# Kernel tuning notes

Measured on AMD Instinct MI355X. Metric: run time of the kernel, lower is better.

The kernel has to match this reference:

```python
import jax, jax.numpy as jnp
import numpy as np

N_NODES = 50000
N_EDGES = 800000
D = 64
IN_DIM = 100
N_GRAPHS = 512
N_LAYERS = 3
OUT_DIM = 24  # n_lbs * n_tasks
BN_EPS = 1e-5


def setup_inputs() -> dict:
    key = jax.random.key(0)
    ks = iter(jax.random.split(key, 40))

    def w(shape):
        fan_in = shape[0]
        return jax.random.normal(next(ks), shape, jnp.float32) / np.float32(np.sqrt(fan_in))

    inp = {}
    inp["x"] = jax.random.normal(next(ks), (N_NODES, IN_DIM), jnp.float32)
    inp["edge_index"] = jax.random.randint(next(ks), (2, N_EDGES), 0, N_NODES, jnp.int32)
    inp["batch"] = jnp.sort(jax.random.randint(next(ks), (N_NODES,), 0, N_GRAPHS, jnp.int32))

    dims_in = [IN_DIM, D, D]
    for i in range(N_LAYERS):
        inp[f"w1_{i}"] = w((dims_in[i], D))
        inp[f"b1_{i}"] = jnp.zeros((D,), jnp.float32)
        inp[f"w2_{i}"] = w((D, D))
        inp[f"b2_{i}"] = jnp.zeros((D,), jnp.float32)

    inp["jk_w"] = w((N_LAYERS * D, D))
    inp["jk_b"] = jnp.zeros((D,), jnp.float32)
    inp["ffn_w1"] = w((D, D))
    inp["ffn_b1"] = jnp.zeros((D,), jnp.float32)
    inp["bn_g"] = jnp.ones((D,), jnp.float32)
    inp["bn_b"] = jnp.zeros((D,), jnp.float32)
    inp["bn_m"] = 0.1 * jax.random.normal(next(ks), (D,), jnp.float32)
    inp["bn_v"] = jax.random.uniform(next(ks), (D,), jnp.float32, 0.5, 1.5)
    inp["ffn_w2"] = w((D, D))
    inp["ffn_b2"] = jnp.zeros((D,), jnp.float32)
    inp["out_w"] = w((D, OUT_DIM))
    inp["out_b"] = jnp.zeros((OUT_DIM,), jnp.float32)
    return inp


def _gin_conv(h, src, dst, w1, b1, w2, b2):
    # sum-aggregate neighbor messages:  agg[dst] += h[src]
    agg = jax.ops.segment_sum(h[src], dst, num_segments=N_NODES)
    z = h + agg  # eps = 0 -> (1 + eps) * x + agg
    # GINConv internal MLP: lin -> relu -> lin (no norm, plain last)
    return jnp.maximum(z @ w1 + b1, 0.0) @ w2 + b2


def reference(x, edge_index, batch,
              w1_0, b1_0, w2_0, b2_0,
              w1_1, b1_1, w2_1, b2_1,
              w1_2, b1_2, w2_2, b2_2,
              jk_w, jk_b,
              ffn_w1, ffn_b1, bn_g, bn_b, bn_m, bn_v, ffn_w2, ffn_b2,
              out_w, out_b):
    src, dst = edge_index[0], edge_index[1]
    layer_params = [(w1_0, b1_0, w2_0, b2_0),
                    (w1_1, b1_1, w2_1, b2_1),
                    (w1_2, b1_2, w2_2, b2_2)]
    xs = []
    h = x
    for (w1, b1, w2, b2) in layer_params:
        h = _gin_conv(h, src, dst, w1, b1, w2, b2)
        h = jnp.maximum(h, 0.0)  # inter-layer ReLU (jk='cat' applies it on every layer)
        xs.append(h)  # dropout is identity in eval
    # JumpingKnowledge 'cat' + final linear -> [N, D]
    h = jnp.concatenate(xs, axis=-1) @ jk_w + jk_b
    # global_add_pool -> [N_GRAPHS, D]
    g = jax.ops.segment_sum(h, batch, num_segments=N_GRAPHS)
    # ffn MLP: lin -> batchnorm (eval, running stats) -> relu -> lin
    t = g @ ffn_w1 + ffn_b1
    t = (t - bn_m) * jax.lax.rsqrt(bn_v + BN_EPS) * bn_g + bn_b
    t = jnp.maximum(t, 0.0) @ ffn_w2 + ffn_b2
    # output layer ('none' uncertainty): plain linear
    logits = t @ out_w + out_b
    return logits
```

## Files before the change

### kernel.cpp

```cpp
#include <hip/hip_runtime.h>

#define NN 50000
#define NE 800000
#define NG 512
#define INDIM 100
#define OUTD 24
#define LROW 72
#define XROW 136
#define CSR_CAP 64
#define NB 196
#define BSH 8
#define BCAP 5120
#define CURS 16
#define EPB 4096
#define B_WPREP 80
#define B_WPREP0 112
#define B_CNT0 308
#define B_GP0 692

typedef __attribute__((ext_vector_type(8))) short short8;
typedef __attribute__((ext_vector_type(4))) float floatx4;

__device__ inline float bf2f(unsigned short u) {
    unsigned v = (unsigned)u << 16;
    float f;
    __builtin_memcpy(&f, &v, 4);
    return f;
}
__device__ inline unsigned short f2bf(float f) {
    unsigned u;
    __builtin_memcpy(&u, &f, 4);
    u += 0x7fffu + ((u >> 16) & 1u);
    return (unsigned short)(u >> 16);
}


__global__ __launch_bounds__(256) void k_prep(const float* __restrict__ s0, const float* __restrict__ s1,
                                              const float* __restrict__ s2, const float* __restrict__ s3,
                                              const float* __restrict__ s4,
                                              const float* __restrict__ w1_0,
                                              unsigned short* __restrict__ wT,
                                              unsigned short* __restrict__ w0T,
                                              int* __restrict__ count,
                                              float* __restrict__ gp,
                                              int* __restrict__ cursor) {
    int b = blockIdx.x, tid = threadIdx.x;
    if (b < B_WPREP) {
        const float* srcs[5] = {s0, s1, s2, s3, s4};
        int id = b >> 4;
        int off = ((b & 15) << 8) + tid;
        int k = off >> 6, n = off & 63;
        wT[id * 4096 + n * 64 + k] = f2bf(srcs[id][k * 64 + n]);
    } else if (b < B_WPREP0) {
        int i = (b - B_WPREP) * 256 + tid;
        int n = i >> 7, k = i & 127;
        w0T[n * 128 + k] = (k < INDIM) ? f2bf(w1_0[k * 64 + n]) : 0;
    } else if (b < B_CNT0) {
        int i = (b - B_WPREP0) * 256 + tid;
        if (i < NN) count[i] = 0;
        if (i < NB * CURS) cursor[i] = 0;
    } else {
        int i = (b - B_CNT0) * 256 + tid;
        if (i < 3 * NG * 64) gp[i] = 0.f;
    }
}


__global__ __launch_bounds__(256) void k_fill_a(const int* __restrict__ ei,
                                                int* __restrict__ cursor,
                                                unsigned* __restrict__ pairs) {
    __shared__ int lcnt[NB];
    __shared__ int lbase[NB];
    int t = threadIdx.x;
    for (int i = t; i < NB; i += 256) lcnt[i] = 0;
    __syncthreads();
    unsigned e0 = blockIdx.x * EPB;
    unsigned short dv[16], sv[16];
    short bkt[16];
#pragma unroll
    for (int j = 0; j < 16; ++j) {
        unsigned e = e0 + j * 256u + t;
        if (e < NE) {
            int d = ei[NE + e];
            int s = ei[e];
            dv[j] = (unsigned short)d;
            sv[j] = (unsigned short)s;
            bkt[j] = (short)(d >> BSH);
            atomicAdd(&lcnt[bkt[j]], 1);
        } else {
            bkt[j] = -1;
        }
    }
    __syncthreads();
    for (int i = t; i < NB; i += 256) {
        lbase[i] = atomicAdd(&cursor[i * CURS], lcnt[i]);
        lcnt[i] = 0;
    }
    __syncthreads();
#pragma unroll
    for (int j = 0; j < 16; ++j) {
        if (bkt[j] >= 0) {
            int b = bkt[j];
            int p = lbase[b] + atomicAdd(&lcnt[b], 1);
            if (p < BCAP)
                pairs[(size_t)b * BCAP + p] = ((unsigned)dv[j] << 16) | (unsigned)sv[j];
        }
    }
}


__global__ __launch_bounds__(256) void k_fill_b(const unsigned* __restrict__ pairs,
                                                const int* __restrict__ cursor,
                                                int* __restrict__ count,
                                                int* __restrict__ csr) {
    __shared__ int lcnt[256];
    int t = threadIdx.x, b = blockIdx.x;
    lcnt[t] = 0;
    __syncthreads();
    int tot = min(cursor[b * CURS], BCAP);
    const unsigned* pp = pairs + (size_t)b * BCAP;
    for (int i = t; i < tot; i += 256) {
        unsigned pr = pp[i];
        int d = (int)(pr >> 16);
        int s = (int)(pr & 0xFFFFu);
        int pos = atomicAdd(&lcnt[d & 255], 1);
        if (pos < CSR_CAP) csr[(size_t)d * CSR_CAP + pos] = s;
    }
    __syncthreads();
    int node = (b << BSH) + t;
    if (node < NN) count[node] = lcnt[t];
}


__global__ __launch_bounds__(256) void k_pre0(const float* __restrict__ x,
                                              const unsigned short* __restrict__ w1T,
                                              unsigned short* __restrict__ y) {
    __shared__ __align__(16) unsigned short xs[64 * XROW];
    int tid = threadIdx.x;
    int base = blockIdx.x * 64;
    for (int i = tid; i < 64 * 128; i += 256) {
        int r = i >> 7, c = i & 127;
        int node = base + r;
        float v = (c < INDIM && node < NN) ? x[(size_t)node * INDIM + c] : 0.f;
        xs[r * XROW + c] = f2bf(v);
    }
    __syncthreads();
    int wave = tid >> 6, lane = tid & 63;
    int quad = lane >> 4, l15 = lane & 15;
#pragma unroll
    for (int nt = 0; nt < 4; ++nt) {
        floatx4 c = {0.f, 0.f, 0.f, 0.f};
#pragma unroll
        for (int kk = 0; kk < 4; ++kk) {
            short8 a = *(const short8*)&xs[(wave * 16 + l15) * XROW + kk * 32 + quad * 8];
            short8 bb = *(const short8*)&w1T[(nt * 16 + l15) * 128 + kk * 32 + quad * 8];
            c = __builtin_amdgcn_mfma_f32_16x16x32_bf16(a, bb, c, 0, 0, 0);
        }
        int col = nt * 16 + l15;
#pragma unroll
        for (int r = 0; r < 4; ++r) {
            int row = base + wave * 16 + quad * 4 + r;
            if (row < NN) y[(size_t)row * 64 + col] = f2bf(c[r]);
        }
    }
}


template <bool HAS_NEXT>
__global__ __launch_bounds__(256) void k_layer(const unsigned short* __restrict__ y,
                                               const int* __restrict__ count,
                                               const int* __restrict__ csr,
                                               const float* __restrict__ b1,
                                               const unsigned short* __restrict__ w2T,
                                               const float* __restrict__ b2,
                                               const unsigned short* __restrict__ wnT,
                                               unsigned short* __restrict__ ynext,
                                               const int* __restrict__ batch,
                                               float* __restrict__ gp) {
    __shared__ __align__(16) unsigned short tA[16 * LROW];
    __shared__ __align__(16) unsigned short tB[16 * LROW];
    int wave = threadIdx.x >> 6, lane = threadIdx.x & 63;
    int base = blockIdx.x * 16;
    float bias1 = b1[lane];

    for (int i = 0; i < 4; i += 2) {
        int nA = __builtin_amdgcn_readfirstlane(base + wave * 4 + i);
        int nB = __builtin_amdgcn_readfirstlane(base + wave * 4 + i + 1);
        int cA = min(count[nA], CSR_CAP);
        int cB = min(count[nB], CSR_CAP);
        const int* pA = csr + (size_t)nA * CSR_CAP;
        const int* pB = csr + (size_t)nB * CSR_CAP;
        float aA[4], aB[4];
        aA[0] = bf2f(y[(size_t)nA * 64 + lane]);
        aB[0] = bf2f(y[(size_t)nB * 64 + lane]);
        aA[1] = aA[2] = aA[3] = 0.f;
        aB[1] = aB[2] = aB[3] = 0.f;
        int eA = 0, eB = 0;
        while (eA + 8 <= cA && eB + 8 <= cB) {
            int iA[8], iB[8];
#pragma unroll
            for (int j = 0; j < 8; ++j) { iA[j] = pA[eA + j]; iB[j] = pB[eB + j]; }
            float vA[8], vB[8];
#pragma unroll
            for (int j = 0; j < 8; ++j) vA[j] = bf2f(y[(size_t)iA[j] * 64 + lane]);
#pragma unroll
            for (int j = 0; j < 8; ++j) vB[j] = bf2f(y[(size_t)iB[j] * 64 + lane]);
#pragma unroll
            for (int j = 0; j < 8; ++j) { aA[j & 3] += vA[j]; aB[j & 3] += vB[j]; }
            eA += 8; eB += 8;
        }
        for (; eA + 8 <= cA; eA += 8) {
            int idx[8];
#pragma unroll
            for (int j = 0; j < 8; ++j) idx[j] = pA[eA + j];
#pragma unroll
            for (int j = 0; j < 8; ++j) aA[j & 3] += bf2f(y[(size_t)idx[j] * 64 + lane]);
        }
        if (eA + 4 <= cA) {
            int i0 = pA[eA], i1 = pA[eA + 1], i2 = pA[eA + 2], i3 = pA[eA + 3];
            aA[0] += bf2f(y[(size_t)i0 * 64 + lane]);
            aA[1] += bf2f(y[(size_t)i1 * 64 + lane]);
            aA[2] += bf2f(y[(size_t)i2 * 64 + lane]);
            aA[3] += bf2f(y[(size_t)i3 * 64 + lane]);
            eA += 4;
        }
        if (eA + 2 <= cA) {
            int i0 = pA[eA], i1 = pA[eA + 1];
            aA[0] += bf2f(y[(size_t)i0 * 64 + lane]);
            aA[1] += bf2f(y[(size_t)i1 * 64 + lane]);
            eA += 2;
        }
        if (eA < cA) aA[0] += bf2f(y[(size_t)pA[eA] * 64 + lane]);
        for (; eB + 8 <= cB; eB += 8) {
            int idx[8];
#pragma unroll
            for (int j = 0; j < 8; ++j) idx[j] = pB[eB + j];
#pragma unroll
            for (int j = 0; j < 8; ++j) aB[j & 3] += bf2f(y[(size_t)idx[j] * 64 + lane]);
        }
        if (eB + 4 <= cB) {
            int i0 = pB[eB], i1 = pB[eB + 1], i2 = pB[eB + 2], i3 = pB[eB + 3];
            aB[0] += bf2f(y[(size_t)i0 * 64 + lane]);
            aB[1] += bf2f(y[(size_t)i1 * 64 + lane]);
            aB[2] += bf2f(y[(size_t)i2 * 64 + lane]);
            aB[3] += bf2f(y[(size_t)i3 * 64 + lane]);
            eB += 4;
        }
        if (eB + 2 <= cB) {
            int i0 = pB[eB], i1 = pB[eB + 1];
            aB[0] += bf2f(y[(size_t)i0 * 64 + lane]);
            aB[1] += bf2f(y[(size_t)i1 * 64 + lane]);
            eB += 2;
        }
        if (eB < cB) aB[0] += bf2f(y[(size_t)pB[eB] * 64 + lane]);

        float sA = (aA[0] + aA[1]) + (aA[2] + aA[3]);
        float sB = (aB[0] + aB[1]) + (aB[2] + aB[3]);
        tA[(wave * 4 + i) * LROW + lane]     = f2bf(fmaxf(sA + bias1, 0.f));
        tA[(wave * 4 + i + 1) * LROW + lane] = f2bf(fmaxf(sB + bias1, 0.f));
    }
    __syncthreads();

    int quad = lane >> 4, l15 = lane & 15;

    short8 a_k0 = *(const short8*)&tA[l15 * LROW + quad * 8];
    short8 a_k1 = *(const short8*)&tA[l15 * LROW + 32 + quad * 8];
    {
        int col = wave * 16 + l15;
        short8 b_k0 = *(const short8*)&w2T[col * 64 + quad * 8];
        short8 b_k1 = *(const short8*)&w2T[col * 64 + 32 + quad * 8];
        floatx4 c = {0.f, 0.f, 0.f, 0.f};
        c = __builtin_amdgcn_mfma_f32_16x16x32_bf16(a_k0, b_k0, c, 0, 0, 0);
        c = __builtin_amdgcn_mfma_f32_16x16x32_bf16(a_k1, b_k1, c, 0, 0, 0);
        float bb = b2[col];
#pragma unroll
        for (int r = 0; r < 4; ++r) {
            float h = fmaxf(c[r] + bb, 0.f);
            tB[(quad * 4 + r) * LROW + col] = f2bf(h);
        }
    }
    __syncthreads();

    if (wave == 0) {
        float run = 0.f;
        int curg = batch[base];
        for (int r = 0; r < 16; ++r) {
            int g2 = batch[base + r];
            if (g2 != curg) {
                atomicAdd(&gp[curg * 64 + lane], run);
                run = 0.f;
                curg = g2;
            }
            run += bf2f(tB[r * LROW + lane]);
        }
        atomicAdd(&gp[curg * 64 + lane], run);
    }

    if (HAS_NEXT) {
        short8 h_k0 = *(const short8*)&tB[l15 * LROW + quad * 8];
        short8 h_k1 = *(const short8*)&tB[l15 * LROW + 32 + quad * 8];
        int col = wave * 16 + l15;
        short8 w_k0 = *(const short8*)&wnT[col * 64 + quad * 8];
        short8 w_k1 = *(const short8*)&wnT[col * 64 + 32 + quad * 8];
        floatx4 cy = {0.f, 0.f, 0.f, 0.f};
        cy = __builtin_amdgcn_mfma_f32_16x16x32_bf16(h_k0, w_k0, cy, 0, 0, 0);
        cy = __builtin_amdgcn_mfma_f32_16x16x32_bf16(h_k1, w_k1, cy, 0, 0, 0);
#pragma unroll
        for (int r = 0; r < 4; ++r) {
            int row = base + quad * 4 + r;
            ynext[(size_t)row * 64 + col] = f2bf(cy[r]);
        }
    }
}


__device__ inline int lbound(const int* __restrict__ b, int v) {
    int lo = 0, hi = NN;
    while (lo < hi) {
        int m = (lo + hi) >> 1;
        if (b[m] < v) lo = m + 1; else hi = m;
    }
    return lo;
}

__global__ __launch_bounds__(64) void k_final(const float* __restrict__ gp,
                                              const int* __restrict__ batch,
                                              const float* __restrict__ jkw,
                                              const float* __restrict__ jkb,
                                              const float* __restrict__ w1,
                                              const float* __restrict__ b1,
                                              const float* __restrict__ bng,
                                              const float* __restrict__ bnb,
                                              const float* __restrict__ bnm,
                                              const float* __restrict__ bnv,
                                              const float* __restrict__ w2,
                                              const float* __restrict__ b2,
                                              const float* __restrict__ ow,
                                              const float* __restrict__ ob,
                                              float* __restrict__ out) {
    __shared__ float gs[192];
    __shared__ float gv[64];
    __shared__ float t2[64];
    __shared__ float t3[64];
    int gr = blockIdx.x, lane = threadIdx.x;
    gs[lane]       = gp[0 * NG * 64 + gr * 64 + lane];
    gs[64 + lane]  = gp[1 * NG * 64 + gr * 64 + lane];
    gs[128 + lane] = gp[2 * NG * 64 + gr * 64 + lane];
    float cntf = (float)(lbound(batch, gr + 1) - lbound(batch, gr));
    __syncthreads();
    float acc = cntf * jkb[lane];
#pragma unroll 8
    for (int k = 0; k < 192; ++k) acc = fmaf(gs[k], jkw[k * 64 + lane], acc);
    gv[lane] = acc;
    __syncthreads();
    acc = b1[lane];
#pragma unroll 8
    for (int k = 0; k < 64; ++k) acc = fmaf(gv[k], w1[k * 64 + lane], acc);
    acc = (acc - bnm[lane]) * rsqrtf(bnv[lane] + 1e-5f) * bng[lane] + bnb[lane];
    t2[lane] = fmaxf(acc, 0.f);
    __syncthreads();
    float acc2 = b2[lane];
#pragma unroll 8
    for (int k = 0; k < 64; ++k) acc2 = fmaf(t2[k], w2[k * 64 + lane], acc2);
    t3[lane] = acc2;
    __syncthreads();
    if (lane < OUTD) {
        float acc3 = ob[lane];
#pragma unroll 8
        for (int k = 0; k < 64; ++k) acc3 = fmaf(t3[k], ow[k * OUTD + lane], acc3);
        out[gr * OUTD + lane] = acc3;
    }
}

extern "C" void kernel_launch(void* const* d_in, const int* in_sizes, int n_in,
                              void* d_out, int out_size, void* d_ws, size_t ws_size,
                              hipStream_t stream) {
    const float* x     = (const float*)d_in[0];
    const int*   ei    = (const int*)d_in[1];
    const int*   batch = (const int*)d_in[2];
    const float* w1_0 = (const float*)d_in[3];
    const float* b1_0 = (const float*)d_in[4];
    const float* w2_0 = (const float*)d_in[5];
    const float* b2_0 = (const float*)d_in[6];
    const float* w1_1 = (const float*)d_in[7];
    const float* b1_1 = (const float*)d_in[8];
    const float* w2_1 = (const float*)d_in[9];
    const float* b2_1 = (const float*)d_in[10];
    const float* w1_2 = (const float*)d_in[11];
    const float* b1_2 = (const float*)d_in[12];
    const float* w2_2 = (const float*)d_in[13];
    const float* b2_2 = (const float*)d_in[14];
    const float* jk_w = (const float*)d_in[15];
    const float* jk_b = (const float*)d_in[16];
    const float* ffn_w1 = (const float*)d_in[17];
    const float* ffn_b1 = (const float*)d_in[18];
    const float* bn_g = (const float*)d_in[19];
    const float* bn_b = (const float*)d_in[20];
    const float* bn_m = (const float*)d_in[21];
    const float* bn_v = (const float*)d_in[22];
    const float* ffn_w2 = (const float*)d_in[23];
    const float* ffn_b2 = (const float*)d_in[24];
    const float* out_w  = (const float*)d_in[25];
    const float* out_b  = (const float*)d_in[26];

    float* ws = (float*)d_ws;
    unsigned short* ya = (unsigned short*)ws;
    unsigned short* yb = ya + 3200000;
    float* gp  = (float*)(yb + 3200000);
    int*   count = (int*)(gp + 3 * NG * 64);
    int*   csr   = count + NN;
    unsigned short* wT  = (unsigned short*)(csr + (size_t)NN * CSR_CAP);
    unsigned short* w0T = wT + 5 * 4096;
    int* cursor = (int*)(w0T + 64 * 128);
    unsigned* pairs = (unsigned*)(cursor + NB * CURS);

    k_prep<<<B_GP0, 256, 0, stream>>>(w2_0, w2_1, w2_2, w1_1, w1_2, w1_0,
                                      wT, w0T, count, gp, cursor);

    k_fill_a<<<(NE + EPB - 1) / EPB, 256, 0, stream>>>(ei, cursor, pairs);
    k_fill_b<<<NB, 256, 0, stream>>>(pairs, cursor, count, csr);

    k_pre0<<<(NN + 63) / 64, 256, 0, stream>>>(x, w0T, ya);

    int nblk = NN / 16;
    k_layer<true><<<nblk, 256, 0, stream>>>(ya, count, csr, b1_0,
                                            wT + 0 * 4096, b2_0, wT + 3 * 4096,
                                            yb, batch, gp + 0 * NG * 64);
    k_layer<true><<<nblk, 256, 0, stream>>>(yb, count, csr, b1_1,
                                            wT + 1 * 4096, b2_1, wT + 4 * 4096,
                                            ya, batch, gp + 1 * NG * 64);
    k_layer<false><<<nblk, 256, 0, stream>>>(ya, count, csr, b1_2,
                                             wT + 2 * 4096, b2_2, nullptr,
                                             nullptr, batch, gp + 2 * NG * 64);

    k_final<<<NG, 64, 0, stream>>>(gp, batch, jk_w, jk_b,
                                   ffn_w1, ffn_b1, bn_g, bn_b, bn_m, bn_v,
                                   ffn_w2, ffn_b2, out_w, out_b, (float*)d_out);
}
```

Measured before the change: 248.0 us.

## Fuse all stages into one persistent cooperative kernel with grid syncs

Replaces the seven separate kernel launches with a single cooperative persistent kernel that uses grid.sync between stages and atomic tile tickets for dynamic work distribution. Edge bucketing (fill_a) and the first-layer projection (pre0) now run in the same phase. The count-array zeroing is dropped because fill_b writes every count. This removes launch overhead and inter-kernel gaps. In exchange it pays for grid barriers, limits occupancy to co-resident blocks sharing one shared-memory footprint, and adds ticket atomics per tile.

```diff
diff --git a/kernel.cpp b/kernel.cpp
--- a/kernel.cpp
+++ b/kernel.cpp
@@ -1,4 +1,5 @@
 #include <hip/hip_runtime.h>
+#include <hip/hip_cooperative_groups.h>
 
 #define NN 50000
 #define NE 800000
@@ -13,13 +14,15 @@
 #define BCAP 5120
 #define CURS 16
 #define EPB 4096
-#define B_WPREP 80
-#define B_WPREP0 112
-#define B_CNT0 308
-#define B_GP0 692
+#define NT_PREP 497
+#define NT_P1 978
+#define NT_LAYER 3125
+#define NT_FINAL 128
 
 typedef __attribute__((ext_vector_type(8))) short short8;
 typedef __attribute__((ext_vector_type(4))) float floatx4;
+
+namespace cg = cooperative_groups;
 
 __device__ inline float bf2f(unsigned short u) {
     unsigned v = (unsigned)u << 16;
@@ -34,55 +37,59 @@
     return (unsigned short)(u >> 16);
 }
 
-
-__global__ __launch_bounds__(256) void k_prep(const float* __restrict__ s0, const float* __restrict__ s1,
-                                              const float* __restrict__ s2, const float* __restrict__ s3,
-                                              const float* __restrict__ s4,
-                                              const float* __restrict__ w1_0,
-                                              unsigned short* __restrict__ wT,
-                                              unsigned short* __restrict__ w0T,
-                                              int* __restrict__ count,
-                                              float* __restrict__ gp,
-                                              int* __restrict__ cursor) {
-    int b = blockIdx.x, tid = threadIdx.x;
-    if (b < B_WPREP) {
-        const float* srcs[5] = {s0, s1, s2, s3, s4};
-        int id = b >> 4;
-        int off = ((b & 15) << 8) + tid;
+struct Params {
+    const float* x;
+    const int* ei;
+    const int* batch;
+    const float *w2_0, *w2_1, *w2_2, *w1_1, *w1_2, *w1_0;
+    const float *b1_0, *b2_0, *b1_1, *b2_1, *b1_2, *b2_2;
+    const float *jkw, *jkb, *fw1, *fb1, *bng, *bnb, *bnm, *bnv, *fw2, *fb2, *ow, *ob;
+    float* out;
+    unsigned short *ya, *yb;
+    float* gp;
+    int* count;
+    int* csr;
+    unsigned short *wT, *w0T;
+    int* cursor;
+    unsigned* pairs;
+    int* tick;
+};
+
+
+__device__ __forceinline__ void prep_body(const Params& p, int u, int tid) {
+    if (u < 80) {
+        const float* srcs[5] = {p.w2_0, p.w2_1, p.w2_2, p.w1_1, p.w1_2};
+        int id = u >> 4;
+        int off = ((u & 15) << 8) + tid;
         int k = off >> 6, n = off & 63;
-        wT[id * 4096 + n * 64 + k] = f2bf(srcs[id][k * 64 + n]);
-    } else if (b < B_WPREP0) {
-        int i = (b - B_WPREP) * 256 + tid;
+        p.wT[id * 4096 + n * 64 + k] = f2bf(srcs[id][k * 64 + n]);
+    } else if (u < 112) {
+        int i = (u - 80) * 256 + tid;
         int n = i >> 7, k = i & 127;
-        w0T[n * 128 + k] = (k < INDIM) ? f2bf(w1_0[k * 64 + n]) : 0;
-    } else if (b < B_CNT0) {
-        int i = (b - B_WPREP0) * 256 + tid;
-        if (i < NN) count[i] = 0;
-        if (i < NB * CURS) cursor[i] = 0;
+        p.w0T[n * 128 + k] = (k < INDIM) ? f2bf(p.w1_0[k * 64 + n]) : 0;
+    } else if (u == 112) {
+        for (int i = tid; i < NB * CURS; i += 256) p.cursor[i] = 0;
+        if (tid < 4) p.tick[tid] = 0;
     } else {
-        int i = (b - B_CNT0) * 256 + tid;
-        if (i < 3 * NG * 64) gp[i] = 0.f;
-    }
-}
-
-
-__global__ __launch_bounds__(256) void k_fill_a(const int* __restrict__ ei,
-                                                int* __restrict__ cursor,
-                                                unsigned* __restrict__ pairs) {
-    __shared__ int lcnt[NB];
-    __shared__ int lbase[NB];
-    int t = threadIdx.x;
-    for (int i = t; i < NB; i += 256) lcnt[i] = 0;
-    __syncthreads();
-    unsigned e0 = blockIdx.x * EPB;
+        int i = (u - 113) * 256 + tid;
+        if (i < 3 * NG * 64) p.gp[i] = 0.f;
+    }
+}
+
+__device__ __forceinline__ void filla_body(const Params& p, int u, int tid, unsigned char* sm) {
+    int* lcnt = (int*)sm;
+    int* lbase = lcnt + NB;
+    for (int i = tid; i < NB; i += 256) lcnt[i] = 0;
+    __syncthreads();
+    unsigned e0 = (unsigned)u * EPB;
     unsigned short dv[16], sv[16];
     short bkt[16];
 #pragma unroll
     for (int j = 0; j < 16; ++j) {
-        unsigned e = e0 + j * 256u + t;
+        unsigned e = e0 + j * 256u + tid;
         if (e < NE) {
-            int d = ei[NE + e];
-            int s = ei[e];
+            int d = p.ei[NE + e];
+            int s = p.ei[e];
             dv[j] = (unsigned short)d;
             sv[j] = (unsigned short)s;
             bkt[j] = (short)(d >> BSH);
@@ -92,8 +99,8 @@
         }
     }
     __syncthreads();
-    for (int i = t; i < NB; i += 256) {
-        lbase[i] = atomicAdd(&cursor[i * CURS], lcnt[i]);
+    for (int i = tid; i < NB; i += 256) {
+        lbase[i] = atomicAdd(&p.cursor[i * CURS], lcnt[i]);
         lcnt[i] = 0;
     }
     __syncthreads();
@@ -101,98 +108,91 @@
     for (int j = 0; j < 16; ++j) {
         if (bkt[j] >= 0) {
             int b = bkt[j];
-            int p = lbase[b] + atomicAdd(&lcnt[b], 1);
-            if (p < BCAP)
-                pairs[(size_t)b * BCAP + p] = ((unsigned)dv[j] << 16) | (unsigned)sv[j];
-        }
-    }
-}
-
-
-__global__ __launch_bounds__(256) void k_fill_b(const unsigned* __restrict__ pairs,
-                                                const int* __restrict__ cursor,
-                                                int* __restrict__ count,
-                                                int* __restrict__ csr) {
-    __shared__ int lcnt[256];
-    int t = threadIdx.x, b = blockIdx.x;
-    lcnt[t] = 0;
-    __syncthreads();
-    int tot = min(cursor[b * CURS], BCAP);
-    const unsigned* pp = pairs + (size_t)b * BCAP;
-    for (int i = t; i < tot; i += 256) {
+            int pos = lbase[b] + atomicAdd(&lcnt[b], 1);
+            if (pos < BCAP)
+                p.pairs[(size_t)b * BCAP + pos] = ((unsigned)dv[j] << 16) | (unsigned)sv[j];
+        }
+    }
+    __syncthreads();
+}
+
+__device__ __forceinline__ void pre0_body(const Params& p, int v, int tid, unsigned char* sm) {
+    unsigned short* xs = (unsigned short*)sm;
+    int base = v * 64;
+    for (int i = tid; i < 64 * 128; i += 256) {
+        int r = i >> 7, c = i & 127;
+        int node = base + r;
+        float val = (c < INDIM && node < NN) ? p.x[(size_t)node * INDIM + c] : 0.f;
+        xs[r * XROW + c] = f2bf(val);
+    }
+    __syncthreads();
+    int wave = tid >> 6, lane = tid & 63;
+    int quad = lane >> 4, l15 = lane & 15;
+#pragma unroll
+    for (int nt = 0; nt < 4; ++nt) {
+        floatx4 c = {0.f, 0.f, 0.f, 0.f};
+#pragma unroll
+        for (int kk = 0; kk < 4; ++kk) {
+            short8 a = *(const short8*)&xs[(wave * 16 + l15) * XROW + kk * 32 + quad * 8];
+            short8 bb = *(const short8*)&p.w0T[(nt * 16 + l15) * 128 + kk * 32 + quad * 8];
+            c = __builtin_amdgcn_mfma_f32_16x16x32_bf16(a, bb, c, 0, 0, 0);
+        }
+        int col = nt * 16 + l15;
+#pragma unroll
+        for (int r = 0; r < 4; ++r) {
+            int row = base + wave * 16 + quad * 4 + r;
+            if (row < NN) p.ya[(size_t)row * 64 + col] = f2bf(c[r]);
+        }
+    }
+    __syncthreads();
+}
+
+__device__ __forceinline__ void fillb_body(const Params& p, int b, int tid, unsigned char* sm) {
+    int* lcnt = (int*)sm;
+    lcnt[tid] = 0;
+    __syncthreads();
+    int tot = min(p.cursor[b * CURS], BCAP);
+    const unsigned* pp = p.pairs + (size_t)b * BCAP;
+    for (int i = tid; i < tot; i += 256) {
         unsigned pr = pp[i];
         int d = (int)(pr >> 16);
         int s = (int)(pr & 0xFFFFu);
         int pos = atomicAdd(&lcnt[d & 255], 1);
-        if (pos < CSR_CAP) csr[(size_t)d * CSR_CAP + pos] = s;
-    }
-    __syncthreads();
-    int node = (b << BSH) + t;
-    if (node < NN) count[node] = lcnt[t];
-}
-
-
-__global__ __launch_bounds__(256) void k_pre0(const float* __restrict__ x,
-                                              const unsigned short* __restrict__ w1T,
-                                              unsigned short* __restrict__ y) {
-    __shared__ __align__(16) unsigned short xs[64 * XROW];
-    int tid = threadIdx.x;
-    int base = blockIdx.x * 64;
-    for (int i = tid; i < 64 * 128; i += 256) {
-        int r = i >> 7, c = i & 127;
-        int node = base + r;
-        float v = (c < INDIM && node < NN) ? x[(size_t)node * INDIM + c] : 0.f;
-        xs[r * XROW + c] = f2bf(v);
-    }
-    __syncthreads();
+        if (pos < CSR_CAP) p.csr[(size_t)d * CSR_CAP + pos] = s;
+    }
+    __syncthreads();
+    int node = (b << BSH) + tid;
+    if (node < NN) p.count[node] = lcnt[tid];
+    __syncthreads();
+}
+
+__device__ __forceinline__ void layer_body(const Params& p, int t, int tid,
+                                           const unsigned short* __restrict__ y,
+                                           const float* __restrict__ b1,
+                                           const unsigned short* __restrict__ w2T,
+                                           const float* __restrict__ b2,
+                                           const unsigned short* __restrict__ wnT,
+                                           unsigned short* __restrict__ ynext,
+                                           float* __restrict__ gp,
+                                           unsigned char* sm) {
+    unsigned short* tA = (unsigned short*)sm;
+    unsigned short* tB = tA + 16 * LROW;
     int wave = tid >> 6, lane = tid & 63;
-    int quad = lane >> 4, l15 = lane & 15;
-#pragma unroll
-    for (int nt = 0; nt < 4; ++nt) {
-        floatx4 c = {0.f, 0.f, 0.f, 0.f};
-#pragma unroll
-        for (int kk = 0; kk < 4; ++kk) {
-            short8 a = *(const short8*)&xs[(wave * 16 + l15) * XROW + kk * 32 + quad * 8];
-            short8 bb = *(const short8*)&w1T[(nt * 16 + l15) * 128 + kk * 32 + quad * 8];
-            c = __builtin_amdgcn_mfma_f32_16x16x32_bf16(a, bb, c, 0, 0, 0);
-        }
-        int col = nt * 16 + l15;
-#pragma unroll
-        for (int r = 0; r < 4; ++r) {
-            int row = base + wave * 16 + quad * 4 + r;
-            if (row < NN) y[(size_t)row * 64 + col] = f2bf(c[r]);
-        }
-    }
-}
-
-
-template <bool HAS_NEXT>
-__global__ __launch_bounds__(256) void k_layer(const unsigned short* __restrict__ y,
-                                               const int* __restrict__ count,
-                                               const int* __restrict__ csr,
-                                               const float* __restrict__ b1,
-                                               const unsigned short* __restrict__ w2T,
-                                               const float* __restrict__ b2,
-                                               const unsigned short* __restrict__ wnT,
-                                               unsigned short* __restrict__ ynext,
-                                               const int* __restrict__ batch,
-                                               float* __restrict__ gp) {
-    __shared__ __align__(16) unsigned short tA[16 * LROW];
-    __shared__ __align__(16) unsigned short tB[16 * LROW];
-    int wave = threadIdx.x >> 6, lane = threadIdx.x & 63;
-    int base = blockIdx.x * 16;
+    int base = t * 16;
     float bias1 = b1[lane];
+    const int* __restrict__ count = p.count;
+    const int* __restrict__ csr = p.csr;
 
     for (int i = 0; i < 4; i += 2) {
         int nA = __builtin_amdgcn_readfirstlane(base + wave * 4 + i);
-        int nB = __builtin_amdgcn_readfirstlane(base + wave * 4 + i + 1);
+        int nBn = __builtin_amdgcn_readfirstlane(base + wave * 4 + i + 1);
         int cA = min(count[nA], CSR_CAP);
-        int cB = min(count[nB], CSR_CAP);
+        int cB = min(count[nBn], CSR_CAP);
         const int* pA = csr + (size_t)nA * CSR_CAP;
-        const int* pB = csr + (size_t)nB * CSR_CAP;
+        const int* pB = csr + (size_t)nBn * CSR_CAP;
         float aA[4], aB[4];
         aA[0] = bf2f(y[(size_t)nA * 64 + lane]);
-        aB[0] = bf2f(y[(size_t)nB * 64 + lane]);
+        aB[0] = bf2f(y[(size_t)nBn * 64 + lane]);
         aA[1] = aA[2] = aA[3] = 0.f;
         aB[1] = aB[2] = aB[3] = 0.f;
         int eA = 0, eB = 0;
@@ -283,9 +283,9 @@
 
     if (wave == 0) {
         float run = 0.f;
-        int curg = batch[base];
+        int curg = p.batch[base];
         for (int r = 0; r < 16; ++r) {
-            int g2 = batch[base + r];
+            int g2 = p.batch[base + r];
             if (g2 != curg) {
                 atomicAdd(&gp[curg * 64 + lane], run);
                 run = 0.f;
@@ -296,7 +296,7 @@
         atomicAdd(&gp[curg * 64 + lane], run);
     }
 
-    if (HAS_NEXT) {
+    if (ynext) {
         short8 h_k0 = *(const short8*)&tB[l15 * LROW + quad * 8];
         short8 h_k1 = *(const short8*)&tB[l15 * LROW + 32 + quad * 8];
         int col = wave * 16 + l15;
@@ -311,8 +311,8 @@
             ynext[(size_t)row * 64 + col] = f2bf(cy[r]);
         }
     }
-}
-
+    __syncthreads();
+}
 
 __device__ inline int lbound(const int* __restrict__ b, int v) {
     int lo = 0, hi = NN;
@@ -323,117 +323,162 @@
     return lo;
 }
 
-__global__ __launch_bounds__(64) void k_final(const float* __restrict__ gp,
-                                              const int* __restrict__ batch,
-                                              const float* __restrict__ jkw,
-                                              const float* __restrict__ jkb,
-                                              const float* __restrict__ w1,
-                                              const float* __restrict__ b1,
-                                              const float* __restrict__ bng,
-                                              const float* __restrict__ bnb,
-                                              const float* __restrict__ bnm,
-                                              const float* __restrict__ bnv,
-                                              const float* __restrict__ w2,
-                                              const float* __restrict__ b2,
-                                              const float* __restrict__ ow,
-                                              const float* __restrict__ ob,
-                                              float* __restrict__ out) {
-    __shared__ float gs[192];
-    __shared__ float gv[64];
-    __shared__ float t2[64];
-    __shared__ float t3[64];
-    int gr = blockIdx.x, lane = threadIdx.x;
-    gs[lane]       = gp[0 * NG * 64 + gr * 64 + lane];
-    gs[64 + lane]  = gp[1 * NG * 64 + gr * 64 + lane];
-    gs[128 + lane] = gp[2 * NG * 64 + gr * 64 + lane];
-    float cntf = (float)(lbound(batch, gr + 1) - lbound(batch, gr));
-    __syncthreads();
-    float acc = cntf * jkb[lane];
+__device__ __forceinline__ void final_body(const Params& p, int u, int tid, unsigned char* sm) {
+    int wave = tid >> 6, lane = tid & 63;
+    int gr = u * 4 + wave;
+    float* gs = (float*)sm + wave * 384;
+    float* gv = gs + 192;
+    float* t2 = gv + 64;
+    float* t3 = t2 + 64;
+    gs[lane]       = p.gp[0 * NG * 64 + gr * 64 + lane];
+    gs[64 + lane]  = p.gp[1 * NG * 64 + gr * 64 + lane];
+    gs[128 + lane] = p.gp[2 * NG * 64 + gr * 64 + lane];
+    float cntf = (float)(lbound(p.batch, gr + 1) - lbound(p.batch, gr));
+    __syncthreads();
+    float acc = cntf * p.jkb[lane];
 #pragma unroll 8
-    for (int k = 0; k < 192; ++k) acc = fmaf(gs[k], jkw[k * 64 + lane], acc);
+    for (int k = 0; k < 192; ++k) acc = fmaf(gs[k], p.jkw[k * 64 + lane], acc);
     gv[lane] = acc;
     __syncthreads();
-    acc = b1[lane];
+    acc = p.fb1[lane];
 #pragma unroll 8
-    for (int k = 0; k < 64; ++k) acc = fmaf(gv[k], w1[k * 64 + lane], acc);
-    acc = (acc - bnm[lane]) * rsqrtf(bnv[lane] + 1e-5f) * bng[lane] + bnb[lane];
+    for (int k = 0; k < 64; ++k) acc = fmaf(gv[k], p.fw1[k * 64 + lane], acc);
+    acc = (acc - p.bnm[lane]) * rsqrtf(p.bnv[lane] + 1e-5f) * p.bng[lane] + p.bnb[lane];
     t2[lane] = fmaxf(acc, 0.f);
     __syncthreads();
-    float acc2 = b2[lane];
+    float acc2 = p.fb2[lane];
 #pragma unroll 8
-    for (int k = 0; k < 64; ++k) acc2 = fmaf(t2[k], w2[k * 64 + lane], acc2);
+    for (int k = 0; k < 64; ++k) acc2 = fmaf(t2[k], p.fw2[k * 64 + lane], acc2);
     t3[lane] = acc2;
     __syncthreads();
     if (lane < OUTD) {
-        float acc3 = ob[lane];
+        float acc3 = p.ob[lane];
 #pragma unroll 8
-        for (int k = 0; k < 64; ++k) acc3 = fmaf(t3[k], ow[k * OUTD + lane], acc3);
-        out[gr * OUTD + lane] = acc3;
-    }
+        for (int k = 0; k < 64; ++k) acc3 = fmaf(t3[k], p.ow[k * OUTD + lane], acc3);
+        p.out[gr * OUTD + lane] = acc3;
+    }
+}
+
+
+__global__ __launch_bounds__(256) void k_all(Params p) {
+    cg::grid_group grid = cg::this_grid();
+    __shared__ __align__(16) unsigned char sm[64 * XROW * 2];
+    __shared__ int sT;
+    int tid = threadIdx.x;
+    int nb = gridDim.x;
+    int bid = blockIdx.x;
+
+    for (int u = bid; u < NT_PREP; u += nb) prep_body(p, u, tid);
+    grid.sync();
+
+    {
+        if (bid < NT_P1) {
+            if (bid < NB) filla_body(p, bid, tid, sm);
+            else pre0_body(p, bid - NB, tid, sm);
+        }
+        if (nb < NT_P1) {
+            for (;;) {
+                __syncthreads();
+                if (tid == 0) sT = nb + atomicAdd(&p.tick[0], 1);
+                __syncthreads();
+                int t2 = sT;
+                if (t2 >= NT_P1) break;
+                if (t2 < NB) filla_body(p, t2, tid, sm);
+                else pre0_body(p, t2 - NB, tid, sm);
+            }
+        }
+    }
+    grid.sync();
+
+    for (int u = bid; u < NB; u += nb) fillb_body(p, u, tid, sm);
+    grid.sync();
+
+#pragma unroll 1
+    for (int l = 0; l < 3; ++l) {
+        const unsigned short* yin = (l == 1) ? p.yb : p.ya;
+        unsigned short* yout = (l == 0) ? p.yb : ((l == 1) ? p.ya : nullptr);
+        const unsigned short* w2T = p.wT + l * 4096;
+        const unsigned short* wnT = p.wT + (3 + l) * 4096;
+        const float* b1 = (l == 0) ? p.b1_0 : (l == 1) ? p.b1_1 : p.b1_2;
+        const float* b2 = (l == 0) ? p.b2_0 : (l == 1) ? p.b2_1 : p.b2_2;
+        float* gp = p.gp + l * NG * 64;
+        if (bid < NT_LAYER)
+            layer_body(p, bid, tid, yin, b1, w2T, b2, wnT, yout, gp, sm);
+        for (;;) {
+            __syncthreads();
+            if (tid == 0) sT = nb + atomicAdd(&p.tick[1 + l], 1);
+            __syncthreads();
+            int t2 = sT;
+            if (t2 >= NT_LAYER) break;
+            layer_body(p, t2, tid, yin, b1, w2T, b2, wnT, yout, gp, sm);
+        }
+        grid.sync();
+    }
+
+    if (bid < NT_FINAL) final_body(p, bid, tid, sm);
 }
 
 extern "C" void kernel_launch(void* const* d_in, const int* in_sizes, int n_in,
                               void* d_out, int out_size, void* d_ws, size_t ws_size,
                               hipStream_t stream) {
-    const float* x     = (const float*)d_in[0];
-    const int*   ei    = (const int*)d_in[1];
-    const int*   batch = (const int*)d_in[2];
-    const float* w1_0 = (const float*)d_in[3];
-    const float* b1_0 = (const float*)d_in[4];
-    const float* w2_0 = (const float*)d_in[5];
-    const float* b2_0 = (const float*)d_in[6];
-    const float* w1_1 = (const float*)d_in[7];
-    const float* b1_1 = (const float*)d_in[8];
-    const float* w2_1 = (const float*)d_in[9];
-    const float* b2_1 = (const float*)d_in[10];
-    const float* w1_2 = (const float*)d_in[11];
-    const float* b1_2 = (const float*)d_in[12];
-    const float* w2_2 = (const float*)d_in[13];
-    const float* b2_2 = (const float*)d_in[14];
-    const float* jk_w = (const float*)d_in[15];
-    const float* jk_b = (const float*)d_in[16];
-    const float* ffn_w1 = (const float*)d_in[17];
-    const float* ffn_b1 = (const float*)d_in[18];
-    const float* bn_g = (const float*)d_in[19];
-    const float* bn_b = (const float*)d_in[20];
-    const float* bn_m = (const float*)d_in[21];
-    const float* bn_v = (const float*)d_in[22];
-    const float* ffn_w2 = (const float*)d_in[23];
-    const float* ffn_b2 = (const float*)d_in[24];
-    const float* out_w  = (const float*)d_in[25];
-    const float* out_b  = (const float*)d_in[26];
+    Params p;
+    p.x     = (const float*)d_in[0];
+    p.ei    = (const int*)d_in[1];
+    p.batch = (const int*)d_in[2];
+    p.w1_0 = (const float*)d_in[3];
+    p.b1_0 = (const float*)d_in[4];
+    p.w2_0 = (const float*)d_in[5];
+    p.b2_0 = (const float*)d_in[6];
+    p.w1_1 = (const float*)d_in[7];
+    p.b1_1 = (const float*)d_in[8];
+    p.w2_1 = (const float*)d_in[9];
+    p.b2_1 = (const float*)d_in[10];
+    p.w1_2 = (const float*)d_in[11];
+    p.b1_2 = (const float*)d_in[12];
+    p.w2_2 = (const float*)d_in[13];
+    p.b2_2 = (const float*)d_in[14];
+    p.jkw  = (const float*)d_in[15];
+    p.jkb  = (const float*)d_in[16];
+    p.fw1  = (const float*)d_in[17];
+    p.fb1  = (const float*)d_in[18];
+    p.bng  = (const float*)d_in[19];
+    p.bnb  = (const float*)d_in[20];
+    p.bnm  = (const float*)d_in[21];
+    p.bnv  = (const float*)d_in[22];
+    p.fw2  = (const float*)d_in[23];
+    p.fb2  = (const float*)d_in[24];
+    p.ow   = (const float*)d_in[25];
+    p.ob   = (const float*)d_in[26];
+    p.out  = (float*)d_out;
 
     float* ws = (float*)d_ws;
-    unsigned short* ya = (unsigned short*)ws;
-    unsigned short* yb = ya + 3200000;
-    float* gp  = (float*)(yb + 3200000);
-    int*   count = (int*)(gp + 3 * NG * 64);
-    int*   csr   = count + NN;
-    unsigned short* wT  = (unsigned short*)(csr + (size_t)NN * CSR_CAP);
-    unsigned short* w0T = wT + 5 * 4096;
-    int* cursor = (int*)(w0T + 64 * 128);
-    unsigned* pairs = (unsigned*)(cursor + NB * CURS);
-
-    k_prep<<<B_GP0, 256, 0, stream>>>(w2_0, w2_1, w2_2, w1_1, w1_2, w1_0,
-                                      wT, w0T, count, gp, cursor);
-
-    k_fill_a<<<(NE + EPB - 1) / EPB, 256, 0, stream>>>(ei, cursor, pairs);
-    k_fill_b<<<NB, 256, 0, stream>>>(pairs, cursor, count, csr);
-
-    k_pre0<<<(NN + 63) / 64, 256, 0, stream>>>(x, w0T, ya);
-
-    int nblk = NN / 16;
-    k_layer<true><<<nblk, 256, 0, stream>>>(ya, count, csr, b1_0,
-                                            wT + 0 * 4096, b2_0, wT + 3 * 4096,
-                                            yb, batch, gp + 0 * NG * 64);
-    k_layer<true><<<nblk, 256, 0, stream>>>(yb, count, csr, b1_1,
-                                            wT + 1 * 4096, b2_1, wT + 4 * 4096,
-                                            ya, batch, gp + 1 * NG * 64);
-    k_layer<false><<<nblk, 256, 0, stream>>>(ya, count, csr, b1_2,
-                                             wT + 2 * 4096, b2_2, nullptr,
-                                             nullptr, batch, gp + 2 * NG * 64);
-
-    k_final<<<NG, 64, 0, stream>>>(gp, batch, jk_w, jk_b,
-                                   ffn_w1, ffn_b1, bn_g, bn_b, bn_m, bn_v,
-                                   ffn_w2, ffn_b2, out_w, out_b, (float*)d_out);
-}
+    p.ya = (unsigned short*)ws;
+    p.yb = p.ya + 3200000;
+    p.gp = (float*)(p.yb + 3200000);
+    p.count = (int*)(p.gp + 3 * NG * 64);
+    p.csr = p.count + NN;
+    p.wT = (unsigned short*)(p.csr + (size_t)NN * CSR_CAP);
+    p.w0T = p.wT + 5 * 4096;
+    p.cursor = (int*)(p.w0T + 64 * 128);
+    p.pairs = (unsigned*)(p.cursor + NB * CURS);
+    p.tick = (int*)(p.pairs + (size_t)NB * BCAP);
+
+    static int nblk_s = 0;
+    if (nblk_s == 0) {
+        int dev = 0;
+        hipGetDevice(&dev);
+        hipDeviceProp_t prop;
+        hipGetDeviceProperties(&prop, dev);
+        int mb = 0;
+        hipOccupancyMaxActiveBlocksPerMultiprocessor(&mb, reinterpret_cast<const void*>(k_all), 256, 0);
+        if (mb < 1) mb = 1;
+        long nb = (long)mb * prop.multiProcessorCount;
+        if (nb > 2048) nb = 2048;
+        if (nb < 256) nb = 256;
+        nblk_s = (int)nb;
+    }
+
+    void* args[] = { (void*)&p };
+    hipLaunchCooperativeKernel(reinterpret_cast<void*>(k_all),
+                               dim3(nblk_s), dim3(256), args, 0, stream);
+}
```

Result: slower. 768.8 us (+210.0%).

## Merge CSR fill with input projection; gather four nodes per wave with zero-row padding

Applied to the files above, without the earlier changes.

Merges the CSR-fill kernel and the first-layer input projection into one launch by giving them disjoint block ranges, which removes a launch and lets the two independent jobs overlap. The per-wave neighbour gather now handles four nodes at once in a single padded loop. Out-of-range slots read a zero row appended at index NN of each feature buffer, replacing the branchy tail code and raising loads in flight. This costs extra wasted loads when degrees within a wave differ, plus more register pressure.

```diff
diff --git a/kernel.cpp b/kernel.cpp
--- a/kernel.cpp
+++ b/kernel.cpp
@@ -8,6 +8,7 @@
 #define LROW 72
 #define XROW 136
 #define CSR_CAP 64
+#define YSZ 3200064
 #define NB 196
 #define BSH 8
 #define BCAP 5120
@@ -43,7 +44,9 @@
                                               unsigned short* __restrict__ w0T,
                                               int* __restrict__ count,
                                               float* __restrict__ gp,
-                                              int* __restrict__ cursor) {
+                                              int* __restrict__ cursor,
+                                              unsigned short* __restrict__ ya,
+                                              unsigned short* __restrict__ yb) {
     int b = blockIdx.x, tid = threadIdx.x;
     if (b < B_WPREP) {
         const float* srcs[5] = {s0, s1, s2, s3, s4};
@@ -59,6 +62,10 @@
         int i = (b - B_WPREP0) * 256 + tid;
         if (i < NN) count[i] = 0;
         if (i < NB * CURS) cursor[i] = 0;
+        if (i < 64) {
+            ya[(size_t)NN * 64 + i] = 0;
+            yb[(size_t)NN * 64 + i] = 0;
+        }
     } else {
         int i = (b - B_CNT0) * 256 + tid;
         if (i < 3 * NG * 64) gp[i] = 0.f;
@@ -109,35 +116,35 @@
 }
 
 
-__global__ __launch_bounds__(256) void k_fill_b(const unsigned* __restrict__ pairs,
-                                                const int* __restrict__ cursor,
-                                                int* __restrict__ count,
-                                                int* __restrict__ csr) {
-    __shared__ int lcnt[256];
-    int t = threadIdx.x, b = blockIdx.x;
-    lcnt[t] = 0;
-    __syncthreads();
-    int tot = min(cursor[b * CURS], BCAP);
-    const unsigned* pp = pairs + (size_t)b * BCAP;
-    for (int i = t; i < tot; i += 256) {
-        unsigned pr = pp[i];
-        int d = (int)(pr >> 16);
-        int s = (int)(pr & 0xFFFFu);
-        int pos = atomicAdd(&lcnt[d & 255], 1);
-        if (pos < CSR_CAP) csr[(size_t)d * CSR_CAP + pos] = s;
-    }
-    __syncthreads();
-    int node = (b << BSH) + t;
-    if (node < NN) count[node] = lcnt[t];
-}
-
-
-__global__ __launch_bounds__(256) void k_pre0(const float* __restrict__ x,
+__global__ __launch_bounds__(256) void k_mid2(const unsigned* __restrict__ pairs,
+                                              const int* __restrict__ cursor,
+                                              int* __restrict__ count,
+                                              int* __restrict__ csr,
+                                              const float* __restrict__ x,
                                               const unsigned short* __restrict__ w1T,
                                               unsigned short* __restrict__ y) {
     __shared__ __align__(16) unsigned short xs[64 * XROW];
     int tid = threadIdx.x;
-    int base = blockIdx.x * 64;
+    if (blockIdx.x < NB) {
+        int* lcnt = (int*)xs;
+        int b = blockIdx.x;
+        lcnt[tid] = 0;
+        __syncthreads();
+        int tot = min(cursor[b * CURS], BCAP);
+        const unsigned* pp = pairs + (size_t)b * BCAP;
+        for (int i = tid; i < tot; i += 256) {
+            unsigned pr = pp[i];
+            int d = (int)(pr >> 16);
+            int s = (int)(pr & 0xFFFFu);
+            int pos = atomicAdd(&lcnt[d & 255], 1);
+            if (pos < CSR_CAP) csr[(size_t)d * CSR_CAP + pos] = s;
+        }
+        __syncthreads();
+        int node = (b << BSH) + tid;
+        if (node < NN) count[node] = lcnt[tid];
+        return;
+    }
+    int base = (blockIdx.x - NB) * 64;
     for (int i = tid; i < 64 * 128; i += 256) {
         int r = i >> 7, c = i & 127;
         int node = base + r;
@@ -183,81 +190,73 @@
     int base = blockIdx.x * 16;
     float bias1 = b1[lane];
 
-    for (int i = 0; i < 4; i += 2) {
-        int nA = __builtin_amdgcn_readfirstlane(base + wave * 4 + i);
-        int nB = __builtin_amdgcn_readfirstlane(base + wave * 4 + i + 1);
-        int cA = min(count[nA], CSR_CAP);
-        int cB = min(count[nB], CSR_CAP);
-        const int* pA = csr + (size_t)nA * CSR_CAP;
-        const int* pB = csr + (size_t)nB * CSR_CAP;
-        float aA[4], aB[4];
-        aA[0] = bf2f(y[(size_t)nA * 64 + lane]);
-        aB[0] = bf2f(y[(size_t)nB * 64 + lane]);
-        aA[1] = aA[2] = aA[3] = 0.f;
-        aB[1] = aB[2] = aB[3] = 0.f;
-        int eA = 0, eB = 0;
-        while (eA + 8 <= cA && eB + 8 <= cB) {
-            int iA[8], iB[8];
-#pragma unroll
-            for (int j = 0; j < 8; ++j) { iA[j] = pA[eA + j]; iB[j] = pB[eB + j]; }
-            float vA[8], vB[8];
-#pragma unroll
-            for (int j = 0; j < 8; ++j) vA[j] = bf2f(y[(size_t)iA[j] * 64 + lane]);
-#pragma unroll
-            for (int j = 0; j < 8; ++j) vB[j] = bf2f(y[(size_t)iB[j] * 64 + lane]);
-#pragma unroll
-            for (int j = 0; j < 8; ++j) { aA[j & 3] += vA[j]; aB[j & 3] += vB[j]; }
-            eA += 8; eB += 8;
-        }
-        for (; eA + 8 <= cA; eA += 8) {
-            int idx[8];
-#pragma unroll
-            for (int j = 0; j < 8; ++j) idx[j] = pA[eA + j];
-#pragma unroll
-            for (int j = 0; j < 8; ++j) aA[j & 3] += bf2f(y[(size_t)idx[j] * 64 + lane]);
-        }
-        if (eA + 4 <= cA) {
-            int i0 = pA[eA], i1 = pA[eA + 1], i2 = pA[eA + 2], i3 = pA[eA + 3];
-            aA[0] += bf2f(y[(size_t)i0 * 64 + lane]);
-            aA[1] += bf2f(y[(size_t)i1 * 64 + lane]);
-            aA[2] += bf2f(y[(size_t)i2 * 64 + lane]);
-            aA[3] += bf2f(y[(size_t)i3 * 64 + lane]);
-            eA += 4;
-        }
-        if (eA + 2 <= cA) {
-            int i0 = pA[eA], i1 = pA[eA + 1];
-            aA[0] += bf2f(y[(size_t)i0 * 64 + lane]);
-            aA[1] += bf2f(y[(size_t)i1 * 64 + lane]);
-            eA += 2;
-        }
-        if (eA < cA) aA[0] += bf2f(y[(size_t)pA[eA] * 64 + lane]);
-        for (; eB + 8 <= cB; eB += 8) {
-            int idx[8];
-#pragma unroll
-            for (int j = 0; j < 8; ++j) idx[j] = pB[eB + j];
-#pragma unroll
-            for (int j = 0; j < 8; ++j) aB[j & 3] += bf2f(y[(size_t)idx[j] * 64 + lane]);
-        }
-        if (eB + 4 <= cB) {
-            int i0 = pB[eB], i1 = pB[eB + 1], i2 = pB[eB + 2], i3 = pB[eB + 3];
-            aB[0] += bf2f(y[(size_t)i0 * 64 + lane]);
-            aB[1] += bf2f(y[(size_t)i1 * 64 + lane]);
-            aB[2] += bf2f(y[(size_t)i2 * 64 + lane]);
-            aB[3] += bf2f(y[(size_t)i3 * 64 + lane]);
-            eB += 4;
-        }
-        if (eB + 2 <= cB) {
-            int i0 = pB[eB], i1 = pB[eB + 1];
-            aB[0] += bf2f(y[(size_t)i0 * 64 + lane]);
-            aB[1] += bf2f(y[(size_t)i1 * 64 + lane]);
-            eB += 2;
-        }
-        if (eB < cB) aB[0] += bf2f(y[(size_t)pB[eB] * 64 + lane]);
-
-        float sA = (aA[0] + aA[1]) + (aA[2] + aA[3]);
-        float sB = (aB[0] + aB[1]) + (aB[2] + aB[3]);
-        tA[(wave * 4 + i) * LROW + lane]     = f2bf(fmaxf(sA + bias1, 0.f));
-        tA[(wave * 4 + i + 1) * LROW + lane] = f2bf(fmaxf(sB + bias1, 0.f));
+    {
+        int nk0 = __builtin_amdgcn_readfirstlane(base + wave * 4 + 0);
+        int nk1 = __builtin_amdgcn_readfirstlane(base + wave * 4 + 1);
+        int nk2 = __builtin_amdgcn_readfirstlane(base + wave * 4 + 2);
+        int nk3 = __builtin_amdgcn_readfirstlane(base + wave * 4 + 3);
+        int ck0 = min(count[nk0], CSR_CAP);
+        int ck1 = min(count[nk1], CSR_CAP);
+        int ck2 = min(count[nk2], CSR_CAP);
+        int ck3 = min(count[nk3], CSR_CAP);
+        const int* pk0 = csr + (size_t)nk0 * CSR_CAP;
+        const int* pk1 = csr + (size_t)nk1 * CSR_CAP;
+        const int* pk2 = csr + (size_t)nk2 * CSR_CAP;
+        const int* pk3 = csr + (size_t)nk3 * CSR_CAP;
+
+        float a0[4], a1[4], a2[4], a3[4];
+        a0[0] = bf2f(y[(size_t)nk0 * 64 + lane]);
+        a1[0] = bf2f(y[(size_t)nk1 * 64 + lane]);
+        a2[0] = bf2f(y[(size_t)nk2 * 64 + lane]);
+        a3[0] = bf2f(y[(size_t)nk3 * 64 + lane]);
+        a0[1] = a0[2] = a0[3] = 0.f;
+        a1[1] = a1[2] = a1[3] = 0.f;
+        a2[1] = a2[2] = a2[3] = 0.f;
+        a3[1] = a3[2] = a3[3] = 0.f;
+
+        int cmax = max(max(ck0, ck1), max(ck2, ck3));
+        int np = (cmax + 7) >> 3;
+        for (int t = 0; t < np; ++t) {
+            int e = t * 8;
+            unsigned short r0[8], r1[8], r2[8], r3[8];
+            int v0 = e < ck0, v1 = e < ck1, v2 = e < ck2, v3 = e < ck3;
+#pragma unroll
+            for (int j = 0; j < 8; ++j) {
+                int i0 = (v0 && e + j < ck0) ? pk0[e + j] : NN;
+                r0[j] = y[(size_t)i0 * 64 + lane];
+            }
+#pragma unroll
+            for (int j = 0; j < 8; ++j) {
+                int i1 = (v1 && e + j < ck1) ? pk1[e + j] : NN;
+                r1[j] = y[(size_t)i1 * 64 + lane];
+            }
+#pragma unroll
+            for (int j = 0; j < 8; ++j) {
+                int i2 = (v2 && e + j < ck2) ? pk2[e + j] : NN;
+                r2[j] = y[(size_t)i2 * 64 + lane];
+            }
+#pragma unroll
+            for (int j = 0; j < 8; ++j) {
+                int i3 = (v3 && e + j < ck3) ? pk3[e + j] : NN;
+                r3[j] = y[(size_t)i3 * 64 + lane];
+            }
+#pragma unroll
+            for (int j = 0; j < 8; ++j) {
+                a0[j & 3] += bf2f(r0[j]);
+                a1[j & 3] += bf2f(r1[j]);
+                a2[j & 3] += bf2f(r2[j]);
+                a3[j & 3] += bf2f(r3[j]);
+            }
+        }
+
+        float s0 = (a0[0] + a0[1]) + (a0[2] + a0[3]);
+        float s1 = (a1[0] + a1[1]) + (a1[2] + a1[3]);
+        float s2 = (a2[0] + a2[1]) + (a2[2] + a2[3]);
+        float s3 = (a3[0] + a3[1]) + (a3[2] + a3[3]);
+        tA[(wave * 4 + 0) * LROW + lane] = f2bf(fmaxf(s0 + bias1, 0.f));
+        tA[(wave * 4 + 1) * LROW + lane] = f2bf(fmaxf(s1 + bias1, 0.f));
+        tA[(wave * 4 + 2) * LROW + lane] = f2bf(fmaxf(s2 + bias1, 0.f));
+        tA[(wave * 4 + 3) * LROW + lane] = f2bf(fmaxf(s3 + bias1, 0.f));
     }
     __syncthreads();
 
@@ -405,8 +404,8 @@
 
     float* ws = (float*)d_ws;
     unsigned short* ya = (unsigned short*)ws;
-    unsigned short* yb = ya + 3200000;
-    float* gp  = (float*)(yb + 3200000);
+    unsigned short* yb = ya + YSZ;
+    float* gp  = (float*)(yb + YSZ);
     int*   count = (int*)(gp + 3 * NG * 64);
     int*   csr   = count + NN;
     unsigned short* wT  = (unsigned short*)(csr + (size_t)NN * CSR_CAP);
@@ -415,12 +414,11 @@
     unsigned* pairs = (unsigned*)(cursor + NB * CURS);
 
     k_prep<<<B_GP0, 256, 0, stream>>>(w2_0, w2_1, w2_2, w1_1, w1_2, w1_0,
-                                      wT, w0T, count, gp, cursor);
+                                      wT, w0T, count, gp, cursor, ya, yb);
 
     k_fill_a<<<(NE + EPB - 1) / EPB, 256, 0, stream>>>(ei, cursor, pairs);
-    k_fill_b<<<NB, 256, 0, stream>>>(pairs, cursor, count, csr);
-
-    k_pre0<<<(NN + 63) / 64, 256, 0, stream>>>(x, w0T, ya);
+
+    k_mid2<<<NB + (NN + 63) / 64, 256, 0, stream>>>(pairs, cursor, count, csr, x, w0T, ya);
 
     int nblk = NN / 16;
     k_layer<true><<<nblk, 256, 0, stream>>>(ya, count, csr, b1_0,
```

New measurement: 276.1 us. +11.3%, slower.
